# Performance work log

Hardware: AMD Instinct MI355X
Metric: run time of the kernel (lower is better)

The kernel has to match this reference:

```python
import jax, jax.numpy as jnp
import numpy as np

N_NODES = 500_000
N_EDGES = 500_000
H = 128  # hidden_channels


def setup_inputs() -> dict:
    key = jax.random.key(0)
    k = jax.random.split(key, 8)
    z = jax.random.normal(k[0], (N_NODES, H), dtype=jnp.float32)
    edge_index = jax.random.randint(k[1], (2, N_EDGES), 0, N_NODES, dtype=jnp.int64)
    s1 = 1.0 / np.sqrt(4 * H)
    s2 = 1.0 / np.sqrt(H)
    s3 = 1.0 / np.sqrt(H // 2)
    W1 = jax.random.uniform(k[2], (4 * H, H), jnp.float32, -s1, s1)
    b1 = jax.random.uniform(k[3], (H,), jnp.float32, -s1, s1)
    W2 = jax.random.uniform(k[4], (H, H // 2), jnp.float32, -s2, s2)
    b2 = jax.random.uniform(k[5], (H // 2,), jnp.float32, -s2, s2)
    W3 = jax.random.uniform(k[6], (H // 2, 1), jnp.float32, -s3, s3)
    b3 = jax.random.uniform(k[7], (1,), jnp.float32, -s3, s3)
    return {"z": z, "edge_index": edge_index,
            "W1": W1, "b1": b1, "W2": W2, "b2": b2, "W3": W3, "b3": b3}


def reference(z, edge_index, W1, b1, W2, b2, W3, b3):
    # gather endpoint embeddings: [E, H]
    src = z[edge_index[0]]
    dst = z[edge_index[1]]
    interaction = src * dst
    difference = jnp.abs(src - dst)
    edge_repr = jnp.concatenate([src, dst, interaction, difference], axis=-1)  # [E, 4H]
    # MLP decoder (dropout = identity at eval)
    h = jax.nn.relu(edge_repr @ W1 + b1)
    h = jax.nn.relu(h @ W2 + b2)
    score = (h @ W3 + b3).squeeze(-1)  # [E]
    return score
```

## Files before the change

### kernel.cpp

```cpp
#include <hip/hip_runtime.h>
#include <stdint.h>


typedef __bf16 bf16x8 __attribute__((ext_vector_type(8)));
typedef __bf16 bf16x4 __attribute__((ext_vector_type(4)));
typedef float  f32x4  __attribute__((ext_vector_type(4)));

__device__ __forceinline__ short f2bf(float f) {
    union { float f; uint32_t u; } v; v.f = f;
    uint32_t u = v.u;
    uint32_t r = (u + 0x7fffu + ((u >> 16) & 1u)) >> 16;
    return (short)r;
}

__device__ __forceinline__ void dma16(const float* gsrc, void* ldst) {
    __builtin_amdgcn_global_load_lds(
        (const __attribute__((address_space(1))) uint32_t*)gsrc,
        (__attribute__((address_space(3))) uint32_t*)ldst,
        16, 0, 0);
}

__global__ void prep_kernel(const float* __restrict__ W1, const float* __restrict__ W2,
                            short* __restrict__ stage1, short* __restrict__ stage2) {
    int idx = blockIdx.x * 256 + threadIdx.x;
    if (idx < 65536) {
        int k = idx >> 7, n = idx & 127;
        float v = W1[idx];
        int ntile = n >> 4, ln = n & 15;
        int kstep = k >> 5, kr = k & 31;
        int lane = (kr >> 3) * 16 + ln;
        int j = kr & 7;
        stage1[(((ntile * 16 + kstep) * 64 + lane) << 3) + j] = f2bf(v);
    } else if (idx < 65536 + 8192) {
        int i2 = idx - 65536;
        int k = i2 >> 6, n = i2 & 63;
        float v = W2[i2];
        int ntile = n >> 4, ln = n & 15;
        int kstep = k >> 5, kr = k & 31;
        int lane = (kr >> 3) * 16 + ln;
        int j = kr & 7;
        stage2[(((ntile * 4 + kstep) * 64 + lane) << 3) + j] = f2bf(v);
    }
}

__launch_bounds__(256, 2)
__global__ void link_kernel(const float* __restrict__ z,
                            const int*   __restrict__ ei,
                            const float* __restrict__ b1,
                            const float* __restrict__ b2,
                            const float* __restrict__ w3,
                            const float* __restrict__ b3,
                            const short* __restrict__ stage1,
                            const short* __restrict__ stage2,
                            float* __restrict__ out,
                            int E) {
    __shared__ __align__(16) char smem[65536];

    const int tid  = threadIdx.x;
    const int lane = tid & 63;
    const int wave = tid >> 6;
    const int ln15 = lane & 15;
    const int quad = lane >> 4;
    const int e0   = blockIdx.x * 64;

    {
        const int hi  = lane >> 5;
        const int ch  = lane & 31;
        const int arr = wave >> 1;
        const int rb  = (wave & 1) * 32;
        int idxs[16];
        #pragma unroll
        for (int i = 0; i < 16; ++i) {
            int e  = rb + 2 * i + hi;
            int eg = e0 + e;
            int egc = eg < E ? eg : (E - 1);
            idxs[i] = ei[arr * E + egc];
        }
        #pragma unroll
        for (int i = 0; i < 16; ++i) {
            const float* src = z + (size_t)idxs[i] * 128 + ch * 4;
            void* dst = smem + (size_t)((wave * 16 + i) * 1024) + lane * 16;
            dma16(src, dst);
        }
    }
    __syncthreads();

    const int c    = tid & 31;
    const int mrow = tid >> 5;
    const int cc   = c >> 1;
    const int half = c & 1;
    f32x4 sv[8], dv[8];
    #pragma unroll
    for (int i = 0; i < 8; ++i) {
        int m = mrow + i * 8;
        sv[i] = *(const f32x4*)(smem + m * 512 + c * 16);
        dv[i] = *(const f32x4*)(smem + 32768 + m * 512 + c * 16);
    }
    __syncthreads();

    #pragma unroll
    for (int i = 0; i < 8; ++i) {
        int m = mrow + i * 8;
        int addr = m * 256 + ((cc ^ (m & 15)) << 4) + half * 8;
        bf16x4 ps, pd;
        #pragma unroll
        for (int j = 0; j < 4; ++j) { ps[j] = (__bf16)sv[i][j]; pd[j] = (__bf16)dv[i][j]; }
        *(bf16x4*)(smem + addr)         = ps;
        *(bf16x4*)(smem + 16384 + addr) = pd;
    }
    __syncthreads();

    f32x4 acc[4][2];
    #pragma unroll
    for (int mt = 0; mt < 4; ++mt)
        #pragma unroll
        for (int nt = 0; nt < 2; ++nt)
            acc[mt][nt] = (f32x4){0.f, 0.f, 0.f, 0.f};

    #pragma unroll
    for (int ks4 = 0; ks4 < 4; ++ks4) {
        bf16x8 Bs[2], Bd[2];
        #pragma unroll
        for (int nt = 0; nt < 2; ++nt) {
            int ntile = wave * 2 + nt;
            Bs[nt] = *(const bf16x8*)(stage1 + (((ntile * 16 + 0 + ks4) * 64 + lane) << 3));
            Bd[nt] = *(const bf16x8*)(stage1 + (((ntile * 16 + 4 + ks4) * 64 + lane) << 3));
        }
        #pragma unroll
        for (int mt = 0; mt < 4; ++mt) {
            int m = mt * 16 + ln15;
            int off = m * 256 + (((ks4 * 4 + quad) ^ (m & 15)) << 4);
            bf16x8 sf = *(const bf16x8*)(smem + off);
            bf16x8 df = *(const bf16x8*)(smem + 16384 + off);
            #pragma unroll
            for (int nt = 0; nt < 2; ++nt) {
                acc[mt][nt] = __builtin_amdgcn_mfma_f32_16x16x32_bf16(sf, Bs[nt], acc[mt][nt], 0, 0, 0);
                acc[mt][nt] = __builtin_amdgcn_mfma_f32_16x16x32_bf16(df, Bd[nt], acc[mt][nt], 0, 0, 0);
            }
        }
    }
    __syncthreads();

    {
        int mder = wave * 16 + ln15;
        #pragma unroll
        for (int ks4 = 0; ks4 < 4; ++ks4) {
            int addr = mder * 256 + (((ks4 * 4 + quad) ^ ln15) << 4);
            bf16x8 s = *(const bf16x8*)(smem + addr);
            bf16x8 d = *(const bf16x8*)(smem + 16384 + addr);
            bf16x8 it, dd;
            #pragma unroll
            for (int j = 0; j < 8; ++j) {
                float fs = (float)s[j], fd = (float)d[j];
                it[j] = (__bf16)(fs * fd);
                dd[j] = (__bf16)__builtin_fabsf(fs - fd);
            }
            *(bf16x8*)(smem + addr)         = it;
            *(bf16x8*)(smem + 16384 + addr) = dd;
        }
    }
    __syncthreads();

    #pragma unroll
    for (int ks4 = 0; ks4 < 4; ++ks4) {
        bf16x8 Bi[2], Bf[2];
        #pragma unroll
        for (int nt = 0; nt < 2; ++nt) {
            int ntile = wave * 2 + nt;
            Bi[nt] = *(const bf16x8*)(stage1 + (((ntile * 16 +  8 + ks4) * 64 + lane) << 3));
            Bf[nt] = *(const bf16x8*)(stage1 + (((ntile * 16 + 12 + ks4) * 64 + lane) << 3));
        }
        #pragma unroll
        for (int mt = 0; mt < 4; ++mt) {
            int m = mt * 16 + ln15;
            int off = m * 256 + (((ks4 * 4 + quad) ^ (m & 15)) << 4);
            bf16x8 itf = *(const bf16x8*)(smem + off);
            bf16x8 ddf = *(const bf16x8*)(smem + 16384 + off);
            #pragma unroll
            for (int nt = 0; nt < 2; ++nt) {
                acc[mt][nt] = __builtin_amdgcn_mfma_f32_16x16x32_bf16(itf, Bi[nt], acc[mt][nt], 0, 0, 0);
                acc[mt][nt] = __builtin_amdgcn_mfma_f32_16x16x32_bf16(ddf, Bf[nt], acc[mt][nt], 0, 0, 0);
            }
        }
    }
    __syncthreads();

    #pragma unroll
    for (int nt = 0; nt < 2; ++nt) {
        int n = (wave * 2 + nt) * 16 + ln15;
        float bias = b1[n];
        #pragma unroll
        for (int mt = 0; mt < 4; ++mt) {
            #pragma unroll
            for (int r = 0; r < 4; ++r) {
                int row = mt * 16 + quad * 4 + r;
                float h = acc[mt][nt][r] + bias;
                h = h > 0.f ? h : 0.f;
                int addr = row * 256 + (((n >> 3) ^ (row & 15)) << 4) + (n & 7) * 2;
                *(short*)(smem + addr) = f2bf(h);
            }
        }
    }
    __syncthreads();

    f32x4 acc2[4];
    #pragma unroll
    for (int mt = 0; mt < 4; ++mt) acc2[mt] = (f32x4){0.f, 0.f, 0.f, 0.f};

    #pragma unroll
    for (int ks = 0; ks < 4; ++ks) {
        bf16x8 b = *(const bf16x8*)(stage2 + (((wave * 4 + ks) * 64 + lane) << 3));
        #pragma unroll
        for (int mt = 0; mt < 4; ++mt) {
            int m = mt * 16 + ln15;
            int ccr = ks * 4 + quad;
            bf16x8 a = *(const bf16x8*)(smem + m * 256 + ((ccr ^ (m & 15)) << 4));
            acc2[mt] = __builtin_amdgcn_mfma_f32_16x16x32_bf16(a, b, acc2[mt], 0, 0, 0);
        }
    }
    __syncthreads();

    {
        int n2 = wave * 16 + ln15;
        float bias = b2[n2];
        #pragma unroll
        for (int mt = 0; mt < 4; ++mt) {
            #pragma unroll
            for (int r = 0; r < 4; ++r) {
                int row = mt * 16 + quad * 4 + r;
                float h = acc2[mt][r] + bias;
                h = h > 0.f ? h : 0.f;
                *(float*)(smem + row * 272 + n2 * 4) = h;
            }
        }
    }
    __syncthreads();

    if (wave == 0) {
        int e = lane;
        float accf = b3[0];
        const float* h2p = (const float*)(smem + e * 272);
        #pragma unroll
        for (int kk = 0; kk < 16; ++kk) {
            f32x4 h = *(const f32x4*)(h2p + kk * 4);
            f32x4 w = *(const f32x4*)(w3 + kk * 4);
            accf += h[0] * w[0] + h[1] * w[1] + h[2] * w[2] + h[3] * w[3];
        }
        if (e0 + e < E) out[e0 + e] = accf;
    }
}

extern "C" void kernel_launch(void* const* d_in, const int* in_sizes, int n_in,
                              void* d_out, int out_size, void* d_ws, size_t ws_size,
                              hipStream_t stream) {
    const float* z  = (const float*)d_in[0];
    const int*   ei = (const int*)  d_in[1];
    const float* W1 = (const float*)d_in[2];
    const float* b1 = (const float*)d_in[3];
    const float* W2 = (const float*)d_in[4];
    const float* b2 = (const float*)d_in[5];
    const float* W3 = (const float*)d_in[6];
    const float* b3 = (const float*)d_in[7];
    float* out = (float*)d_out;

    int E = in_sizes[1] / 2;

    short* stage1 = (short*)d_ws;
    short* stage2 = stage1 + 65536;

    prep_kernel<<<288, 256, 0, stream>>>(W1, W2, stage1, stage2);

    int nblk = (E + 63) / 64;
    link_kernel<<<nblk, 256, 0, stream>>>(z, ei, b1, b2, W3, b3, stage1, stage2, out, E);
}
```

Measured before the change: 468.0 us.

## Halve LDS footprint by staging src and dst gathers sequentially

The src and dst endpoint gathers now share one 32 KB LDS buffer and run one after the other instead of filling a 64 KB buffer together. Launch bounds move from 2 to 4 blocks per CU so more blocks can be resident to hide gather latency. In exchange the two gathers no longer overlap inside a block, extra barriers are added, and the register cap per thread is tighter, which may cause spills.

```diff
diff --git a/kernel.cpp b/kernel.cpp
--- a/kernel.cpp
+++ b/kernel.cpp
@@ -43,7 +43,7 @@
     }
 }
 
-__launch_bounds__(256, 2)
+__launch_bounds__(256, 4)
 __global__ void link_kernel(const float* __restrict__ z,
                             const int*   __restrict__ ei,
                             const float* __restrict__ b1,
@@ -54,7 +54,7 @@
                             const short* __restrict__ stage2,
                             float* __restrict__ out,
                             int E) {
-    __shared__ __align__(16) char smem[65536];
+    __shared__ __align__(16) char smem[32768];
 
     const int tid  = threadIdx.x;
     const int lane = tid & 63;
@@ -63,38 +63,58 @@
     const int quad = lane >> 4;
     const int e0   = blockIdx.x * 64;
 
-    {
-        const int hi  = lane >> 5;
-        const int ch  = lane & 31;
-        const int arr = wave >> 1;
-        const int rb  = (wave & 1) * 32;
-        int idxs[16];
-        #pragma unroll
-        for (int i = 0; i < 16; ++i) {
-            int e  = rb + 2 * i + hi;
-            int eg = e0 + e;
-            int egc = eg < E ? eg : (E - 1);
-            idxs[i] = ei[arr * E + egc];
-        }
-        #pragma unroll
-        for (int i = 0; i < 16; ++i) {
-            const float* src = z + (size_t)idxs[i] * 128 + ch * 4;
-            void* dst = smem + (size_t)((wave * 16 + i) * 1024) + lane * 16;
-            dma16(src, dst);
-        }
-    }
-    __syncthreads();
-
     const int c    = tid & 31;
     const int mrow = tid >> 5;
     const int cc   = c >> 1;
     const int half = c & 1;
+    const int hi   = lane >> 5;
+    const int ch   = lane & 31;
+
     f32x4 sv[8], dv[8];
+
+    {
+        int idxs[8];
+        #pragma unroll
+        for (int i = 0; i < 8; ++i) {
+            int eg  = e0 + wave * 16 + 2 * i + hi;
+            int egc = eg < E ? eg : (E - 1);
+            idxs[i] = ei[egc];
+        }
+        #pragma unroll
+        for (int i = 0; i < 8; ++i) {
+            const float* src = z + (size_t)idxs[i] * 128 + ch * 4;
+            void* dst = smem + (wave * 8192 + i * 1024) + lane * 16;
+            dma16(src, dst);
+        }
+    }
+    __syncthreads();
     #pragma unroll
     for (int i = 0; i < 8; ++i) {
         int m = mrow + i * 8;
         sv[i] = *(const f32x4*)(smem + m * 512 + c * 16);
-        dv[i] = *(const f32x4*)(smem + 32768 + m * 512 + c * 16);
+    }
+    __syncthreads();
+
+    {
+        int idxs[8];
+        #pragma unroll
+        for (int i = 0; i < 8; ++i) {
+            int eg  = e0 + wave * 16 + 2 * i + hi;
+            int egc = eg < E ? eg : (E - 1);
+            idxs[i] = ei[E + egc];
+        }
+        #pragma unroll
+        for (int i = 0; i < 8; ++i) {
+            const float* src = z + (size_t)idxs[i] * 128 + ch * 4;
+            void* dst = smem + (wave * 8192 + i * 1024) + lane * 16;
+            dma16(src, dst);
+        }
+    }
+    __syncthreads();
+    #pragma unroll
+    for (int i = 0; i < 8; ++i) {
+        int m = mrow + i * 8;
+        dv[i] = *(const f32x4*)(smem + m * 512 + c * 16);
     }
     __syncthreads();
 
```

Result: faster. 427.1 us (-8.7%).
